# Kernel tuning notes

Hardware: AMD Instinct MI355X
Metric: run time of the kernel (lower is better)

The kernel has to match this reference:

```python
import jax, jax.numpy as jnp
import numpy as np

HIDDEN = 2048
NUM_HEADS = 16
HEAD_DIM = HIDDEN // NUM_HEADS
REWARD_DIM = 1
B, S = 2, 2048


def setup_inputs() -> dict:
    key = jax.random.key(0)
    ks = jax.random.split(key, 16)
    std = 0.02
    inp = {
        "query": jax.random.normal(ks[0], (B, S, HIDDEN), jnp.float32),
        "key": jax.random.normal(ks[1], (B, S, HIDDEN), jnp.float32),
        "value": jax.random.normal(ks[2], (B, S, HIDDEN), jnp.float32),
        "rewards": jax.random.normal(ks[3], (B, S, REWARD_DIM), jnp.float32),
        "attention_mask": jnp.ones((B, S), dtype=bool),
        # linear params stored as (in, out); apply as x @ W + b
        "Wq": jax.random.normal(ks[4], (HIDDEN, HIDDEN), jnp.float32) * std,
        "bq": jnp.zeros((HIDDEN,), jnp.float32),
        "Wk": jax.random.normal(ks[5], (HIDDEN, HIDDEN), jnp.float32) * std,
        "bk": jnp.zeros((HIDDEN,), jnp.float32),
        "Wv": jax.random.normal(ks[6], (HIDDEN, HIDDEN), jnp.float32) * std,
        "bv": jnp.zeros((HIDDEN,), jnp.float32),
        "Wo": jax.random.normal(ks[7], (HIDDEN, HIDDEN), jnp.float32) * std,
        "bo": jnp.zeros((HIDDEN,), jnp.float32),
        "Wr": jax.random.normal(ks[8], (REWARD_DIM, HIDDEN), jnp.float32) * std,
        "br": jnp.zeros((HIDDEN,), jnp.float32),
        "Wa": jax.random.normal(ks[9], (HIDDEN, NUM_HEADS), jnp.float32) * std,
        "ba": jnp.zeros((NUM_HEADS,), jnp.float32),
    }
    return inp


def reference(query, key, value, rewards, attention_mask,
              Wq, bq, Wk, bk, Wv, bv, Wo, bo, Wr, br, Wa, ba):
    b, s, h = query.shape
    nh, hd = NUM_HEADS, HEAD_DIM
    scale = hd ** -0.5

    q = (query @ Wq + bq).reshape(b, s, nh, hd).transpose(0, 2, 1, 3)  # [b,nh,s,hd]
    k = (key @ Wk + bk).reshape(b, s, nh, hd).transpose(0, 2, 1, 3)
    v = (value @ Wv + bv).reshape(b, s, nh, hd).transpose(0, 2, 1, 3)

    # reward-conditioned per-(batch, head, query) additive bias
    reward_features = rewards @ Wr + br           # [b,s,hidden]
    reward_bias = reward_features @ Wa + ba        # [b,s,nh]
    reward_bias = reward_bias.transpose(0, 2, 1)[..., None]  # [b,nh,s,1]

    scores = jnp.einsum("bhqd,bhkd->bhqk", q, k) * scale + reward_bias
    scores = jnp.where(attention_mask[:, None, None, :], scores, -1e9)

    attention_weights = jax.nn.softmax(scores, axis=-1)        # [b,nh,s,s]
    attended = jnp.einsum("bhqk,bhkd->bqhd", attention_weights, v)
    attended = attended.reshape(b, s, h)
    output = attended @ Wo + bo
    return output, attention_weights.mean(axis=1)
```

## Files before the change

### kernel.cpp

```cpp
#include <hip/hip_runtime.h>

typedef unsigned short u16;
typedef __attribute__((ext_vector_type(8))) short bf16x8;
typedef __attribute__((ext_vector_type(8))) unsigned short u16x8;
typedef __attribute__((ext_vector_type(4))) float f32x4;

#define MFMA16(a, b, c) __builtin_amdgcn_mfma_f32_16x16x32_bf16((a), (b), (c), 0, 0, 0)
#define QSCALE (0.08838834764831845f * 1.4426950408889634f)

#define GLDS(l, g) __builtin_amdgcn_global_load_lds((const __attribute__((address_space(1))) void*)(g), \
                                                    (__attribute__((address_space(3))) void*)(l), 16, 0, 0)

__device__ __forceinline__ u16 f2bf(float f) {
    union { float f; unsigned int u; } x; x.f = f;
    unsigned int lsb = (x.u >> 16) & 1u;
    return (u16)((x.u + 0x7FFFu + lsb) >> 16);
}
__device__ __forceinline__ float exp2v(float x) {
    return __builtin_amdgcn_exp2f(x);
}

__global__ __launch_bounds__(256) void cvt_k(const float* __restrict__ in, u16* __restrict__ out) {
    const size_t stride = (size_t)gridDim.x * 2048;
    for (size_t i = ((size_t)blockIdx.x * 256 + threadIdx.x) * 8; i < 8388608; i += stride) {
        f32x4 a = *(const f32x4*)(in + i);
        f32x4 b = *(const f32x4*)(in + i + 4);
        u16x8 p;
#pragma unroll
        for (int j = 0; j < 4; j++) { p[j] = f2bf(a[j]); p[4 + j] = f2bf(b[j]); }
        *(u16x8*)(out + i) = p;
    }
}

__global__ __launch_bounds__(256) void transpose_k(const float* __restrict__ W, u16* __restrict__ WT) {
    __shared__ u16 tile[128][136];
    const int tid = threadIdx.x;
    const int k0 = blockIdx.y * 128, n0 = blockIdx.x * 128;
#pragma unroll
    for (int i = 0; i < 16; i++) {
        int idx = tid + i * 256;
        int r = idx >> 5, c4 = (idx & 31) * 4;
        f32x4 v = *(const f32x4*)(W + (size_t)(k0 + r) * 2048 + n0 + c4);
#pragma unroll
        for (int j = 0; j < 4; j++) tile[c4 + j][r] = f2bf(v[j]);
    }
    __syncthreads();
#pragma unroll
    for (int i = 0; i < 8; i++) {
        int idx = tid + i * 256;
        int r = idx >> 4, c = (idx & 15) * 8;
        *(u16x8*)(WT + (size_t)(n0 + r) * 2048 + k0 + c) = *(const u16x8*)&tile[r][c];
    }
}

__global__ __launch_bounds__(256) void repack_k(const u16* __restrict__ RM, u16* __restrict__ P) {
    const int bh = blockIdx.y, s0 = blockIdx.x * 128;
    const int b = bh >> 4, h = bh & 15;
    const u16* src = RM + (size_t)(b * 2048 + s0) * 2048 + h * 128;
    u16* dst = P + (size_t)bh * 262144 + (size_t)s0 * 128;
    const int tid = threadIdx.x;
#pragma unroll
    for (int i = 0; i < 8; i++) {
        int idx = tid + i * 256;
        int r = idx >> 4, c = (idx & 15) * 8;
        *(u16x8*)(dst + (size_t)r * 128 + c) = *(const u16x8*)(src + (size_t)r * 2048 + c);
    }
}

__global__ __launch_bounds__(256) void vt_k(const u16* __restrict__ V, u16* __restrict__ VT) {
    const int bh = blockIdx.y, s0 = blockIdx.x * 128;
    const int b = bh >> 4, h = bh & 15;
    const u16* src = V + (size_t)(b * 2048 + s0) * 2048 + h * 128;
    u16* dst = VT + (size_t)bh * 262144 + s0;
    const int bi = threadIdx.x >> 4;
    const int bj = threadIdx.x & 15;
    u16x8 v[8];
#pragma unroll
    for (int r = 0; r < 8; r++) v[r] = *(const u16x8*)(src + (size_t)(bi * 8 + r) * 2048 + bj * 8);
#pragma unroll
    for (int c = 0; c < 8; c++) {
        u16x8 t;
#pragma unroll
        for (int r = 0; r < 8; r++) t[r] = v[r][c];
        *(u16x8*)(dst + (size_t)(bj * 8 + c) * 2048 + bi * 8) = t;
    }
}

template <int F32OUT>
__global__ __launch_bounds__(256) void gemm_k(const u16* __restrict__ A, const u16* __restrict__ WT,
                                              const float* __restrict__ bias, void* __restrict__ Cv,
                                              float scale) {
    __shared__ __align__(16) u16 sh[17408];
    const int tid = threadIdx.x;
    const int wave = tid >> 6, lane = tid & 63;
    const int wm = wave >> 1, wn = wave & 1;
    const int quad = lane >> 4, l15 = lane & 15;
    const int m0 = blockIdx.y * 128, n0 = blockIdx.x * 128;

    const u16* aPtr[2]; const u16* bPtr[2]; int sOff[2];
#pragma unroll
    for (int i = 0; i < 2; i++) {
        int ck = i * 4 + wave;
        int r = ck * 16 + (lane >> 2);
        int ce = (lane & 3) * 8;
        aPtr[i] = A + (size_t)(m0 + r) * 2048 + ce;
        bPtr[i] = WT + (size_t)(n0 + r) * 2048 + ce;
        sOff[i] = ck * 512;
    }
    f32x4 acc[4][4];
#pragma unroll
    for (int a = 0; a < 4; a++)
#pragma unroll
        for (int b = 0; b < 4; b++) acc[a][b] = (f32x4){0.f, 0.f, 0.f, 0.f};

#pragma unroll
    for (int i = 0; i < 2; i++) {
        GLDS(sh + sOff[i], aPtr[i]);
        GLDS(sh + 4096 + sOff[i], bPtr[i]);
        aPtr[i] += 32; bPtr[i] += 32;
    }
    __syncthreads();

    int cur = 0;
    for (int k0 = 0; k0 < 2048; k0 += 32) {
        if (k0 < 2016) {
            u16* db = sh + (cur ^ 1) * 8192;
#pragma unroll
            for (int i = 0; i < 2; i++) {
                GLDS(db + sOff[i], aPtr[i]);
                GLDS(db + 4096 + sOff[i], bPtr[i]);
                aPtr[i] += 32; bPtr[i] += 32;
            }
        }
        const u16* As = sh + cur * 8192;
        const u16* Bs = As + 4096;
        bf16x8 af[4], bfv[4];
#pragma unroll
        for (int mt = 0; mt < 4; mt++) af[mt] = *(const bf16x8*)&As[(wm * 64 + mt * 16 + l15) * 32 + quad * 8];
#pragma unroll
        for (int nt = 0; nt < 4; nt++) bfv[nt] = *(const bf16x8*)&Bs[(wn * 64 + nt * 16 + l15) * 32 + quad * 8];
#pragma unroll
        for (int mt = 0; mt < 4; mt++)
#pragma unroll
            for (int nt = 0; nt < 4; nt++) acc[mt][nt] = MFMA16(af[mt], bfv[nt], acc[mt][nt]);
        __syncthreads();
        cur ^= 1;
    }

    float bv[4];
#pragma unroll
    for (int nt = 0; nt < 4; nt++) bv[nt] = bias[n0 + wn * 64 + nt * 16 + l15];

    if (F32OUT) {
        float* C = (float*)Cv;
#pragma unroll
        for (int mt = 0; mt < 4; mt++) {
            int rb = wm * 64 + mt * 16 + quad * 4;
#pragma unroll
            for (int nt = 0; nt < 4; nt++) {
                int col = n0 + wn * 64 + nt * 16 + l15;
#pragma unroll
                for (int reg = 0; reg < 4; reg++)
                    C[(size_t)(m0 + rb + reg) * 2048 + col] = acc[mt][nt][reg] + bv[nt];
            }
        }
    } else {
        u16* Ot = sh;
#pragma unroll
        for (int mt = 0; mt < 4; mt++) {
            int rb = wm * 64 + mt * 16 + quad * 4;
#pragma unroll
            for (int nt = 0; nt < 4; nt++) {
                int cl = wn * 64 + nt * 16 + l15;
#pragma unroll
                for (int reg = 0; reg < 4; reg++)
                    Ot[(rb + reg) * 136 + cl] = f2bf((acc[mt][nt][reg] + bv[nt]) * scale);
            }
        }
        __syncthreads();
        u16* C = (u16*)Cv;
#pragma unroll
        for (int i = 0; i < 8; i++) {
            int idx = tid + i * 256, r = idx >> 4, c = (idx & 15) * 8;
            *(u16x8*)(C + (size_t)(m0 + r) * 2048 + n0 + c) = *(const u16x8*)&Ot[r * 136 + c];
        }
    }
}

__global__ __launch_bounds__(256) void flash2_k(const u16* __restrict__ Q, const u16* __restrict__ K,
                                                const u16* __restrict__ VT, u16* __restrict__ att,
                                                float* __restrict__ ML) {
    __shared__ __align__(16) u16 sh[64 * 144 + 128 * 80];
    u16* Ks = sh;
    u16* Vs = sh + 64 * 144;

    const int tid = threadIdx.x;
    const int wave = tid >> 6, lane = tid & 63;
    const int quad = lane >> 4, l15 = lane & 15;
    const int bh = blockIdx.x & 31;
    const int q0 = (blockIdx.x >> 5) * 128;
    const size_t ho = (size_t)bh * 262144;
    const int qw = wave * 32;

    bf16x8 bq[2][4];
#pragma unroll
    for (int nt = 0; nt < 2; nt++)
#pragma unroll
        for (int df = 0; df < 4; df++)
            bq[nt][df] = *(const bf16x8*)(Q + ho + (size_t)(q0 + qw + nt * 16 + l15) * 128 + df * 32 + quad * 8);

    f32x4 acc[8][2];
#pragma unroll
    for (int a = 0; a < 8; a++)
#pragma unroll
        for (int b = 0; b < 2; b++) acc[a][b] = (f32x4){0.f, 0.f, 0.f, 0.f};
    float m_[2] = {-1e30f, -1e30f}, l_[2] = {0.f, 0.f};

    for (int kt = 0; kt < 32; kt++) {
        __syncthreads();
#pragma unroll
        for (int i = 0; i < 4; i++) {
            int idx = tid + i * 256, r = idx >> 4, c = (idx & 15) * 8;
            *(u16x8*)&Ks[r * 144 + c] = *(const u16x8*)(K + ho + (size_t)(kt * 64 + r) * 128 + c);
        }
#pragma unroll
        for (int i = 0; i < 4; i++) {
            int idx = tid + i * 256, d = idx >> 3, u = idx & 7;
            *(u16x8*)&Vs[d * 80 + u * 8] = *(const u16x8*)(VT + ho + (size_t)d * 2048 + kt * 64 + u * 8);
        }
        __syncthreads();

        f32x4 st[4][2];
#pragma unroll
        for (int t = 0; t < 4; t++)
#pragma unroll
            for (int nt = 0; nt < 2; nt++) st[t][nt] = (f32x4){0.f, 0.f, 0.f, 0.f};
#pragma unroll
        for (int df = 0; df < 4; df++) {
#pragma unroll
            for (int t = 0; t < 4; t++) {
                bf16x8 ak = *(const bf16x8*)&Ks[(t * 16 + l15) * 144 + df * 32 + quad * 8];
                st[t][0] = MFMA16(ak, bq[0][df], st[t][0]);
                st[t][1] = MFMA16(ak, bq[1][df], st[t][1]);
            }
        }

        float corr[2];
        int pw[4][2][2];
#pragma unroll
        for (int nt = 0; nt < 2; nt++) {
            float tm = -1e30f;
#pragma unroll
            for (int t = 0; t < 4; t++)
#pragma unroll
                for (int reg = 0; reg < 4; reg++) tm = fmaxf(tm, st[t][nt][reg]);
            tm = fmaxf(tm, __shfl_xor(tm, 16));
            tm = fmaxf(tm, __shfl_xor(tm, 32));
            float mn = fmaxf(m_[nt], tm);
            corr[nt] = exp2v(m_[nt] - mn);
            m_[nt] = mn;
            float cs = 0.f;
#pragma unroll
            for (int t = 0; t < 4; t++) {
                float p0 = exp2v(st[t][nt][0] - mn);
                float p1 = exp2v(st[t][nt][1] - mn);
                float p2 = exp2v(st[t][nt][2] - mn);
                float p3 = exp2v(st[t][nt][3] - mn);
                cs += (p0 + p1) + (p2 + p3);
                pw[t][nt][0] = (int)f2bf(p0) | ((int)f2bf(p1) << 16);
                pw[t][nt][1] = (int)f2bf(p2) | ((int)f2bf(p3) << 16);
            }
            cs += __shfl_xor(cs, 16);
            cs += __shfl_xor(cs, 32);
            l_[nt] = l_[nt] * corr[nt] + cs;
        }
#pragma unroll
        for (int mt = 0; mt < 8; mt++)
#pragma unroll
            for (int nt = 0; nt < 2; nt++) {
                acc[mt][nt][0] *= corr[nt]; acc[mt][nt][1] *= corr[nt];
                acc[mt][nt][2] *= corr[nt]; acc[mt][nt][3] *= corr[nt];
            }

        const int s0l = 32 * (quad & 1) + l15, s1l = s0l + 16;
        const bool hi = quad >= 2;
#pragma unroll
        for (int kf = 0; kf < 2; kf++) {
            bf16x8 bp[2];
#pragma unroll
            for (int nt = 0; nt < 2; nt++) {
                int tA = kf * 2, tB = kf * 2 + 1;
                int a0A = __shfl(pw[tA][nt][0], s0l), a0B = __shfl(pw[tB][nt][0], s0l);
                int a1A = __shfl(pw[tA][nt][1], s0l), a1B = __shfl(pw[tB][nt][1], s0l);
                int a2A = __shfl(pw[tA][nt][0], s1l), a2B = __shfl(pw[tB][nt][0], s1l);
                int a3A = __shfl(pw[tA][nt][1], s1l), a3B = __shfl(pw[tB][nt][1], s1l);
                union { int w[4]; bf16x8 v; } u;
                u.w[0] = hi ? a0B : a0A;
                u.w[1] = hi ? a1B : a1A;
                u.w[2] = hi ? a2B : a2A;
                u.w[3] = hi ? a3B : a3A;
                bp[nt] = u.v;
            }
#pragma unroll
            for (int mt = 0; mt < 8; mt++) {
                bf16x8 av = *(const bf16x8*)&Vs[(mt * 16 + l15) * 80 + kf * 32 + quad * 8];
                acc[mt][0] = MFMA16(av, bp[0], acc[mt][0]);
                acc[mt][1] = MFMA16(av, bp[1], acc[mt][1]);
            }
        }
    }

    if (quad == 0) {
#pragma unroll
        for (int nt = 0; nt < 2; nt++)
            ML[(size_t)bh * 2048 + q0 + qw + nt * 16 + l15] = m_[nt] + __log2f(l_[nt]);
    }

    __syncthreads();
    u16* Ot = Ks;
    float inv0 = 1.f / l_[0], inv1 = 1.f / l_[1];
#pragma unroll
    for (int mt = 0; mt < 8; mt++)
#pragma unroll
        for (int reg = 0; reg < 4; reg++) {
            int d = mt * 16 + quad * 4 + reg;
            Ot[(qw + l15) * 136 + d] = f2bf(acc[mt][0][reg] * inv0);
            Ot[(qw + 16 + l15) * 136 + d] = f2bf(acc[mt][1][reg] * inv1);
        }
    __syncthreads();
    const int bB = bh >> 4, h = bh & 15;
    u16* attBase = att + (size_t)(bB * 2048 + q0) * 2048 + h * 128;
#pragma unroll
    for (int i = 0; i < 8; i++) {
        int idx = tid + i * 256, r = idx >> 4, c = (idx & 15) * 8;
        *(u16x8*)(attBase + (size_t)r * 2048 + c) = *(const u16x8*)&Ot[r * 136 + c];
    }
}

__global__ __launch_bounds__(256) void meanw_k(const u16* __restrict__ Q, const u16* __restrict__ K,
                                               const float* __restrict__ ML, float* __restrict__ W2) {
    __shared__ __align__(16) u16 Ks[128][136];
    __shared__ float ml_s[64];
    const int tid = threadIdx.x;
    const int wave = tid >> 6, lane = tid & 63;
    const int wm = wave >> 1, wn = wave & 1;
    const int quad = lane >> 4, l15 = lane & 15;
    const int k0 = blockIdx.x * 128, q0 = blockIdx.y * 64, bb = blockIdx.z;

    f32x4 macc[2][4];
#pragma unroll
    for (int a = 0; a < 2; a++)
#pragma unroll
        for (int b = 0; b < 4; b++) macc[a][b] = (f32x4){0.f, 0.f, 0.f, 0.f};

    for (int h = 0; h < 16; h++) {
        __syncthreads();
        const size_t ho = (size_t)(bb * 16 + h) * 262144;
        const u16* kb = K + ho + (size_t)k0 * 128;
#pragma unroll
        for (int i = 0; i < 8; i++) {
            int idx = tid + i * 256;
            int rr = idx >> 4, c = (idx & 15) * 8;
            *(u16x8*)&Ks[rr][c] = *(const u16x8*)(kb + (size_t)rr * 128 + c);
        }
        if (tid < 64) ml_s[tid] = ML[(size_t)(bb * 16 + h) * 2048 + q0 + tid];
        __syncthreads();
        const u16* qb = Q + ho + (size_t)q0 * 128;
        bf16x8 aq[2][4];
#pragma unroll
        for (int mt = 0; mt < 2; mt++)
#pragma unroll
            for (int ks = 0; ks < 4; ks++)
                aq[mt][ks] = *(const bf16x8*)(qb + (size_t)(wm * 32 + mt * 16 + l15) * 128 + ks * 32 + quad * 8);
#pragma unroll
        for (int mt = 0; mt < 2; mt++) {
            int rb = wm * 32 + mt * 16 + quad * 4;
#pragma unroll
            for (int nt = 0; nt < 4; nt++) {
                f32x4 s4 = (f32x4){0.f, 0.f, 0.f, 0.f};
#pragma unroll
                for (int ks = 0; ks < 4; ks++) {
                    bf16x8 bk = *(const bf16x8*)&Ks[wn * 64 + nt * 16 + l15][ks * 32 + quad * 8];
                    s4 = MFMA16(aq[mt][ks], bk, s4);
                }
#pragma unroll
                for (int reg = 0; reg < 4; reg++)
                    macc[mt][nt][reg] += exp2v(s4[reg] - ml_s[rb + reg]);
            }
        }
    }
#pragma unroll
    for (int mt = 0; mt < 2; mt++) {
        int rb = wm * 32 + mt * 16 + quad * 4;
#pragma unroll
        for (int nt = 0; nt < 4; nt++) {
            int col = k0 + wn * 64 + nt * 16 + l15;
#pragma unroll
            for (int reg = 0; reg < 4; reg++) {
                int row = q0 + rb + reg;
                W2[((size_t)bb * 2048 + row) * 2048 + col] = macc[mt][nt][reg] * 0.0625f;
            }
        }
    }
}

extern "C" void kernel_launch(void* const* d_in, const int* in_sizes, int n_in,
                              void* d_out, int out_size, void* d_ws, size_t ws_size,
                              hipStream_t stream) {
    (void)in_sizes; (void)n_in; (void)out_size; (void)ws_size;
    const float* query = (const float*)d_in[0];
    const float* key   = (const float*)d_in[1];
    const float* value = (const float*)d_in[2];
    const float* Wq = (const float*)d_in[5];
    const float* bq = (const float*)d_in[6];
    const float* Wk = (const float*)d_in[7];
    const float* bk = (const float*)d_in[8];
    const float* Wv = (const float*)d_in[9];
    const float* bv = (const float*)d_in[10];
    const float* Wo = (const float*)d_in[11];
    const float* bo = (const float*)d_in[12];

    float* out1 = (float*)d_out;
    float* out2 = out1 + (size_t)2 * 2048 * 2048;

    u16* qt  = (u16*)d_ws;
    u16* ktw = qt + (size_t)8388608;
    u16* WoT = ktw + (size_t)8388608;
    float* MLb = (float*)(WoT + (size_t)4194304);
    u16* Wt1 = (u16*)out1;
    u16* qb  = Wt1 + (size_t)4194304;
    u16* att = (u16*)out2;
    u16* vtT = att + (size_t)8388608;

    dim3 tg(16, 16);
    dim3 gg(16, 32);
    dim3 rp(16, 32);

    cvt_k<<<2048, 256, 0, stream>>>(query, qb);
    transpose_k<<<tg, 256, 0, stream>>>(Wq, Wt1);
    gemm_k<0><<<gg, 256, 0, stream>>>(qb, Wt1, bq, vtT, (float)QSCALE);
    repack_k<<<rp, 256, 0, stream>>>(vtT, qt);

    cvt_k<<<2048, 256, 0, stream>>>(key, qb);
    transpose_k<<<tg, 256, 0, stream>>>(Wk, Wt1);
    gemm_k<0><<<gg, 256, 0, stream>>>(qb, Wt1, bk, vtT, 1.f);
    repack_k<<<rp, 256, 0, stream>>>(vtT, ktw);

    cvt_k<<<2048, 256, 0, stream>>>(value, qb);
    transpose_k<<<tg, 256, 0, stream>>>(Wv, Wt1);
    gemm_k<0><<<gg, 256, 0, stream>>>(qb, Wt1, bv, att, 1.f);
    vt_k<<<dim3(16, 32), 256, 0, stream>>>(att, vtT);

    flash2_k<<<512, 256, 0, stream>>>(qt, ktw, vtT, att, MLb);

    transpose_k<<<tg, 256, 0, stream>>>(Wo, WoT);
    gemm_k<1><<<gg, 256, 0, stream>>>(att, WoT, bo, out1, 1.f);

    meanw_k<<<dim3(16, 32, 2), 256, 0, stream>>>(qt, ktw, MLb, out2);
}
```

Measured before the change: 645.1 us.

## Batch QKV projections, fuse fp32 conversion and head repack, lazy softmax rescale

The three weight transposes become one launch, and the three Q/K/V projection GEMMs become one batched launch. That GEMM reads the fp32 activations directly, converts them to bf16 while staging into shared memory, and writes Q and K straight into per-head packed layout. This removes the separate conversion and repack kernels and their extra global memory traffic. In flash attention, the running max and the rescaling of the accumulator are now skipped unless the new tile max exceeds the old one by more than 8 (log2 units). That saves exp and multiply work but lets intermediate exponentials grow up to 2^8 before they are rescaled.

```diff
diff --git a/kernel.cpp b/kernel.cpp
--- a/kernel.cpp
+++ b/kernel.cpp
@@ -3,6 +3,7 @@
 typedef unsigned short u16;
 typedef __attribute__((ext_vector_type(8))) short bf16x8;
 typedef __attribute__((ext_vector_type(8))) unsigned short u16x8;
+typedef __attribute__((ext_vector_type(4))) unsigned short u16x4;
 typedef __attribute__((ext_vector_type(4))) float f32x4;
 
 #define MFMA16(a, b, c) __builtin_amdgcn_mfma_f32_16x16x32_bf16((a), (b), (c), 0, 0, 0)
@@ -20,15 +21,28 @@
     return __builtin_amdgcn_exp2f(x);
 }
 
-__global__ __launch_bounds__(256) void cvt_k(const float* __restrict__ in, u16* __restrict__ out) {
-    const size_t stride = (size_t)gridDim.x * 2048;
-    for (size_t i = ((size_t)blockIdx.x * 256 + threadIdx.x) * 8; i < 8388608; i += stride) {
-        f32x4 a = *(const f32x4*)(in + i);
-        f32x4 b = *(const f32x4*)(in + i + 4);
-        u16x8 p;
-#pragma unroll
-        for (int j = 0; j < 4; j++) { p[j] = f2bf(a[j]); p[4 + j] = f2bf(b[j]); }
-        *(u16x8*)(out + i) = p;
+__global__ __launch_bounds__(256) void transpose3_k(const float* __restrict__ W0, const float* __restrict__ W1,
+                                                    const float* __restrict__ W2, u16* __restrict__ T0,
+                                                    u16* __restrict__ T1, u16* __restrict__ T2) {
+    const float* W = blockIdx.z == 0 ? W0 : blockIdx.z == 1 ? W1 : W2;
+    u16* WT = blockIdx.z == 0 ? T0 : blockIdx.z == 1 ? T1 : T2;
+    __shared__ u16 tile[128][136];
+    const int tid = threadIdx.x;
+    const int k0 = blockIdx.y * 128, n0 = blockIdx.x * 128;
+#pragma unroll
+    for (int i = 0; i < 16; i++) {
+        int idx = tid + i * 256;
+        int r = idx >> 5, c4 = (idx & 31) * 4;
+        f32x4 v = *(const f32x4*)(W + (size_t)(k0 + r) * 2048 + n0 + c4);
+#pragma unroll
+        for (int j = 0; j < 4; j++) tile[c4 + j][r] = f2bf(v[j]);
+    }
+    __syncthreads();
+#pragma unroll
+    for (int i = 0; i < 8; i++) {
+        int idx = tid + i * 256;
+        int r = idx >> 4, c = (idx & 15) * 8;
+        *(u16x8*)(WT + (size_t)(n0 + r) * 2048 + k0 + c) = *(const u16x8*)&tile[r][c];
     }
 }
 
@@ -50,20 +64,6 @@
         int idx = tid + i * 256;
         int r = idx >> 4, c = (idx & 15) * 8;
         *(u16x8*)(WT + (size_t)(n0 + r) * 2048 + k0 + c) = *(const u16x8*)&tile[r][c];
-    }
-}
-
-__global__ __launch_bounds__(256) void repack_k(const u16* __restrict__ RM, u16* __restrict__ P) {
-    const int bh = blockIdx.y, s0 = blockIdx.x * 128;
-    const int b = bh >> 4, h = bh & 15;
-    const u16* src = RM + (size_t)(b * 2048 + s0) * 2048 + h * 128;
-    u16* dst = P + (size_t)bh * 262144 + (size_t)s0 * 128;
-    const int tid = threadIdx.x;
-#pragma unroll
-    for (int i = 0; i < 8; i++) {
-        int idx = tid + i * 256;
-        int r = idx >> 4, c = (idx & 15) * 8;
-        *(u16x8*)(dst + (size_t)r * 128 + c) = *(const u16x8*)(src + (size_t)r * 2048 + c);
     }
 }
 
@@ -86,11 +86,126 @@
     }
 }
 
-template <int F32OUT>
-__global__ __launch_bounds__(256) void gemm_k(const u16* __restrict__ A, const u16* __restrict__ WT,
-                                              const float* __restrict__ bias, void* __restrict__ Cv,
-                                              float scale) {
+__global__ __launch_bounds__(256) void gemm_p(const float* __restrict__ A0, const float* __restrict__ A1,
+                                              const float* __restrict__ A2, const u16* __restrict__ W0,
+                                              const u16* __restrict__ W1, const u16* __restrict__ W2,
+                                              const float* __restrict__ b0, const float* __restrict__ b1,
+                                              const float* __restrict__ b2, u16* __restrict__ C0,
+                                              u16* __restrict__ C1, u16* __restrict__ C2) {
+    const int z = blockIdx.z;
+    const float* A = z == 0 ? A0 : z == 1 ? A1 : A2;
+    const u16* WT = z == 0 ? W0 : z == 1 ? W1 : W2;
+    const float* bias = z == 0 ? b0 : z == 1 ? b1 : b2;
+    u16* C = z == 0 ? C0 : z == 1 ? C1 : C2;
+    const float scale = z == 0 ? (float)QSCALE : 1.f;
+
     __shared__ __align__(16) u16 sh[17408];
+    const int tid = threadIdx.x;
+    const int wave = tid >> 6, lane = tid & 63;
+    const int wm = wave >> 1, wn = wave & 1;
+    const int quad = lane >> 4, l15 = lane & 15;
+    const int m0 = blockIdx.y * 128, n0 = blockIdx.x * 128;
+
+    const float* aBase = A + (size_t)(m0 + (tid >> 3)) * 2048 + (tid & 7) * 4;
+    const int aOff = (tid >> 3) * 32 + (tid & 7) * 4;
+    const u16* bPtr[2]; int sOff[2];
+#pragma unroll
+    for (int i = 0; i < 2; i++) {
+        int ck = i * 4 + wave;
+        int r = ck * 16 + (lane >> 2);
+        bPtr[i] = WT + (size_t)(n0 + r) * 2048 + (lane & 3) * 8;
+        sOff[i] = ck * 512;
+    }
+    f32x4 acc[4][4];
+#pragma unroll
+    for (int a = 0; a < 4; a++)
+#pragma unroll
+        for (int b = 0; b < 4; b++) acc[a][b] = (f32x4){0.f, 0.f, 0.f, 0.f};
+
+#pragma unroll
+    for (int i = 0; i < 4; i++) {
+        f32x4 v = *(const f32x4*)(aBase + (size_t)i * 32 * 2048);
+        u16x4 p;
+#pragma unroll
+        for (int j = 0; j < 4; j++) p[j] = f2bf(v[j]);
+        *(u16x4*)&sh[aOff + i * 1024] = p;
+    }
+#pragma unroll
+    for (int i = 0; i < 2; i++) {
+        GLDS(sh + 4096 + sOff[i], bPtr[i]);
+        bPtr[i] += 32;
+    }
+    __syncthreads();
+
+    int cur = 0;
+    for (int k0 = 0; k0 < 2048; k0 += 32) {
+        if (k0 < 2016) {
+            u16* db = sh + (cur ^ 1) * 8192;
+#pragma unroll
+            for (int i = 0; i < 4; i++) {
+                f32x4 v = *(const f32x4*)(aBase + (size_t)i * 32 * 2048 + k0 + 32);
+                u16x4 p;
+#pragma unroll
+                for (int j = 0; j < 4; j++) p[j] = f2bf(v[j]);
+                *(u16x4*)&db[aOff + i * 1024] = p;
+            }
+#pragma unroll
+            for (int i = 0; i < 2; i++) {
+                GLDS(db + 4096 + sOff[i], bPtr[i]);
+                bPtr[i] += 32;
+            }
+        }
+        const u16* As = sh + cur * 8192;
+        const u16* Bs = As + 4096;
+        bf16x8 af[4], bfv[4];
+#pragma unroll
+        for (int mt = 0; mt < 4; mt++) af[mt] = *(const bf16x8*)&As[(wm * 64 + mt * 16 + l15) * 32 + quad * 8];
+#pragma unroll
+        for (int nt = 0; nt < 4; nt++) bfv[nt] = *(const bf16x8*)&Bs[(wn * 64 + nt * 16 + l15) * 32 + quad * 8];
+#pragma unroll
+        for (int mt = 0; mt < 4; mt++)
+#pragma unroll
+            for (int nt = 0; nt < 4; nt++) acc[mt][nt] = MFMA16(af[mt], bfv[nt], acc[mt][nt]);
+        __syncthreads();
+        cur ^= 1;
+    }
+
+    float bv[4];
+#pragma unroll
+    for (int nt = 0; nt < 4; nt++) bv[nt] = bias[n0 + wn * 64 + nt * 16 + l15];
+
+    u16* Ot = sh;
+#pragma unroll
+    for (int mt = 0; mt < 4; mt++) {
+        int rb = wm * 64 + mt * 16 + quad * 4;
+#pragma unroll
+        for (int nt = 0; nt < 4; nt++) {
+            int cl = wn * 64 + nt * 16 + l15;
+#pragma unroll
+            for (int reg = 0; reg < 4; reg++)
+                Ot[(rb + reg) * 136 + cl] = f2bf((acc[mt][nt][reg] + bv[nt]) * scale);
+        }
+    }
+    __syncthreads();
+    if (z < 2) {
+        u16* dst = C + ((size_t)((m0 >> 11) * 16 + (n0 >> 7)) * 2048 + (m0 & 2047)) * 128;
+#pragma unroll
+        for (int i = 0; i < 8; i++) {
+            int idx = tid + i * 256, r = idx >> 4, c = (idx & 15) * 8;
+            *(u16x8*)(dst + (size_t)r * 128 + c) = *(const u16x8*)&Ot[r * 136 + c];
+        }
+    } else {
+#pragma unroll
+        for (int i = 0; i < 8; i++) {
+            int idx = tid + i * 256, r = idx >> 4, c = (idx & 15) * 8;
+            *(u16x8*)(C + (size_t)(m0 + r) * 2048 + n0 + c) = *(const u16x8*)&Ot[r * 136 + c];
+        }
+    }
+}
+
+__global__ __launch_bounds__(256) void gemm_o(const u16* __restrict__ A, const u16* __restrict__ WT,
+                                              const float* __restrict__ bias, float* __restrict__ C) {
+    __shared__ __align__(16) u16 sh[16384];
     const int tid = threadIdx.x;
     const int wave = tid >> 6, lane = tid & 63;
     const int wm = wave >> 1, wn = wave & 1;
@@ -150,39 +265,15 @@
     float bv[4];
 #pragma unroll
     for (int nt = 0; nt < 4; nt++) bv[nt] = bias[n0 + wn * 64 + nt * 16 + l15];
-
-    if (F32OUT) {
-        float* C = (float*)Cv;
-#pragma unroll
-        for (int mt = 0; mt < 4; mt++) {
-            int rb = wm * 64 + mt * 16 + quad * 4;
-#pragma unroll
-            for (int nt = 0; nt < 4; nt++) {
-                int col = n0 + wn * 64 + nt * 16 + l15;
-#pragma unroll
-                for (int reg = 0; reg < 4; reg++)
-                    C[(size_t)(m0 + rb + reg) * 2048 + col] = acc[mt][nt][reg] + bv[nt];
-            }
-        }
-    } else {
-        u16* Ot = sh;
-#pragma unroll
-        for (int mt = 0; mt < 4; mt++) {
-            int rb = wm * 64 + mt * 16 + quad * 4;
-#pragma unroll
-            for (int nt = 0; nt < 4; nt++) {
-                int cl = wn * 64 + nt * 16 + l15;
-#pragma unroll
-                for (int reg = 0; reg < 4; reg++)
-                    Ot[(rb + reg) * 136 + cl] = f2bf((acc[mt][nt][reg] + bv[nt]) * scale);
-            }
-        }
-        __syncthreads();
-        u16* C = (u16*)Cv;
-#pragma unroll
-        for (int i = 0; i < 8; i++) {
-            int idx = tid + i * 256, r = idx >> 4, c = (idx & 15) * 8;
-            *(u16x8*)(C + (size_t)(m0 + r) * 2048 + n0 + c) = *(const u16x8*)&Ot[r * 136 + c];
+#pragma unroll
+    for (int mt = 0; mt < 4; mt++) {
+        int rb = wm * 64 + mt * 16 + quad * 4;
+#pragma unroll
+        for (int nt = 0; nt < 4; nt++) {
+            int col = n0 + wn * 64 + nt * 16 + l15;
+#pragma unroll
+            for (int reg = 0; reg < 4; reg++)
+                C[(size_t)(m0 + rb + reg) * 2048 + col] = acc[mt][nt][reg] + bv[nt];
         }
     }
 }
@@ -245,42 +336,53 @@
             }
         }
 
-        float corr[2];
+        float tm[2];
+#pragma unroll
+        for (int nt = 0; nt < 2; nt++) {
+            float x = -1e30f;
+#pragma unroll
+            for (int t = 0; t < 4; t++)
+#pragma unroll
+                for (int reg = 0; reg < 4; reg++) x = fmaxf(x, st[t][nt][reg]);
+            x = fmaxf(x, __shfl_xor(x, 16));
+            x = fmaxf(x, __shfl_xor(x, 32));
+            tm[nt] = x;
+        }
+        if (!__all(fmaxf(tm[0] - m_[0], tm[1] - m_[1]) <= 8.f)) {
+            float corr[2];
+#pragma unroll
+            for (int nt = 0; nt < 2; nt++) {
+                float mn = fmaxf(m_[nt], tm[nt]);
+                corr[nt] = exp2v(m_[nt] - mn);
+                m_[nt] = mn;
+                l_[nt] *= corr[nt];
+            }
+#pragma unroll
+            for (int mt = 0; mt < 8; mt++)
+#pragma unroll
+                for (int nt = 0; nt < 2; nt++) {
+                    acc[mt][nt][0] *= corr[nt]; acc[mt][nt][1] *= corr[nt];
+                    acc[mt][nt][2] *= corr[nt]; acc[mt][nt][3] *= corr[nt];
+                }
+        }
         int pw[4][2][2];
 #pragma unroll
         for (int nt = 0; nt < 2; nt++) {
-            float tm = -1e30f;
-#pragma unroll
-            for (int t = 0; t < 4; t++)
-#pragma unroll
-                for (int reg = 0; reg < 4; reg++) tm = fmaxf(tm, st[t][nt][reg]);
-            tm = fmaxf(tm, __shfl_xor(tm, 16));
-            tm = fmaxf(tm, __shfl_xor(tm, 32));
-            float mn = fmaxf(m_[nt], tm);
-            corr[nt] = exp2v(m_[nt] - mn);
-            m_[nt] = mn;
             float cs = 0.f;
 #pragma unroll
             for (int t = 0; t < 4; t++) {
-                float p0 = exp2v(st[t][nt][0] - mn);
-                float p1 = exp2v(st[t][nt][1] - mn);
-                float p2 = exp2v(st[t][nt][2] - mn);
-                float p3 = exp2v(st[t][nt][3] - mn);
+                float p0 = exp2v(st[t][nt][0] - m_[nt]);
+                float p1 = exp2v(st[t][nt][1] - m_[nt]);
+                float p2 = exp2v(st[t][nt][2] - m_[nt]);
+                float p3 = exp2v(st[t][nt][3] - m_[nt]);
                 cs += (p0 + p1) + (p2 + p3);
                 pw[t][nt][0] = (int)f2bf(p0) | ((int)f2bf(p1) << 16);
                 pw[t][nt][1] = (int)f2bf(p2) | ((int)f2bf(p3) << 16);
             }
             cs += __shfl_xor(cs, 16);
             cs += __shfl_xor(cs, 32);
-            l_[nt] = l_[nt] * corr[nt] + cs;
-        }
-#pragma unroll
-        for (int mt = 0; mt < 8; mt++)
-#pragma unroll
-            for (int nt = 0; nt < 2; nt++) {
-                acc[mt][nt][0] *= corr[nt]; acc[mt][nt][1] *= corr[nt];
-                acc[mt][nt][2] *= corr[nt]; acc[mt][nt][3] *= corr[nt];
-            }
+            l_[nt] += cs;
+        }
 
         const int s0l = 32 * (quad & 1) + l15, s1l = s0l + 16;
         const bool hi = quad >= 2;
@@ -427,34 +529,20 @@
     u16* ktw = qt + (size_t)8388608;
     u16* WoT = ktw + (size_t)8388608;
     float* MLb = (float*)(WoT + (size_t)4194304);
-    u16* Wt1 = (u16*)out1;
-    u16* qb  = Wt1 + (size_t)4194304;
+    u16* WTq = (u16*)out1;
+    u16* WTk = WTq + (size_t)4194304;
+    u16* WTv = WTk + (size_t)4194304;
     u16* att = (u16*)out2;
     u16* vtT = att + (size_t)8388608;
 
-    dim3 tg(16, 16);
-    dim3 gg(16, 32);
-    dim3 rp(16, 32);
-
-    cvt_k<<<2048, 256, 0, stream>>>(query, qb);
-    transpose_k<<<tg, 256, 0, stream>>>(Wq, Wt1);
-    gemm_k<0><<<gg, 256, 0, stream>>>(qb, Wt1, bq, vtT, (float)QSCALE);
-    repack_k<<<rp, 256, 0, stream>>>(vtT, qt);
-
-    cvt_k<<<2048, 256, 0, stream>>>(key, qb);
-    transpose_k<<<tg, 256, 0, stream>>>(Wk, Wt1);
-    gemm_k<0><<<gg, 256, 0, stream>>>(qb, Wt1, bk, vtT, 1.f);
-    repack_k<<<rp, 256, 0, stream>>>(vtT, ktw);
-
-    cvt_k<<<2048, 256, 0, stream>>>(value, qb);
-    transpose_k<<<tg, 256, 0, stream>>>(Wv, Wt1);
-    gemm_k<0><<<gg, 256, 0, stream>>>(qb, Wt1, bv, att, 1.f);
+    transpose3_k<<<dim3(16, 16, 3), 256, 0, stream>>>(Wq, Wk, Wv, WTq, WTk, WTv);
+    gemm_p<<<dim3(16, 32, 3), 256, 0, stream>>>(query, key, value, WTq, WTk, WTv,
+                                                bq, bk, bv, qt, ktw, att );
     vt_k<<<dim3(16, 32), 256, 0, stream>>>(att, vtT);
-
     flash2_k<<<512, 256, 0, stream>>>(qt, ktw, vtT, att, MLb);
 
-    transpose_k<<<tg, 256, 0, stream>>>(Wo, WoT);
-    gemm_k<1><<<gg, 256, 0, stream>>>(att, WoT, bo, out1, 1.f);
+    transpose_k<<<dim3(16, 16), 256, 0, stream>>>(Wo, WoT);
+    gemm_o<<<dim3(16, 32), 256, 0, stream>>>(att, WoT, bo, out1);
 
     meanw_k<<<dim3(16, 32, 2), 256, 0, stream>>>(qt, ktw, MLb, out2);
 }
```

Measured after the change: 692.0 us. 7.3% more time.
